# Kernel tuning notes

Measured on AMD Instinct MI355X. Metric: run time of the kernel, lower is better.

Reference implementation:

```python
import jax, jax.numpy as jnp
import numpy as np

LEVELS = [5023, 1256, 314, 79, 20]  # mesh vertex counts, fine -> coarse
T = 64        # number of audio frames
LATENT = 128  # latent_channels
S = 9         # spiral length
OUT_CH = [32, 64, 64, 128]


def setup_inputs() -> dict:
    key = jax.random.key(0)
    ks = list(jax.random.split(key, 40))
    nk = lambda: ks.pop()
    inp = {}
    inp["latent"] = jax.random.normal(nk(), (T, LATENT), jnp.float32)
    inp["actor"] = jax.random.normal(nk(), (LEVELS[0], 3), jnp.float32)
    # spiral indices per mesh level (levels 0..3 carry SpiralConvs)
    for l in range(4):
        n = LEVELS[l]
        inp[f"spiral{l}"] = jax.random.randint(nk(), (n, S), 0, n)
    # sparse up-transforms: level l+1 (coarse) -> level l (fine), ~3 nnz per fine vertex
    for l in range(4):
        nf, nc = LEVELS[l], LEVELS[l + 1]
        nnz = 3 * nf
        inp[f"up{l}_rows"] = jax.random.randint(nk(), (nnz,), 0, nf)
        inp[f"up{l}_cols"] = jax.random.randint(nk(), (nnz,), 0, nc)
        inp[f"up{l}_vals"] = jax.random.uniform(nk(), (nnz,), jnp.float32)
    def lin(k, od, idim):
        scale = np.sqrt(2.0 / (od + idim)).astype(np.float32)  # xavier-uniform-ish std
        return jax.random.normal(k, (od, idim), jnp.float32) * scale
    # de_layers[0]: Linear(latent -> num_vert * out_channels[-1])
    inp["W0"] = lin(nk(), LEVELS[4] * OUT_CH[-1], LATENT)
    inp["b0"] = jnp.zeros((LEVELS[4] * OUT_CH[-1],), jnp.float32)
    # SpiralDeblock convs (coarse -> fine): 128->128, 128->64, 64->64, 64->32
    inp["W1"] = lin(nk(), 128, 128 * S); inp["b1"] = jnp.zeros((128,), jnp.float32)
    inp["W2"] = lin(nk(), 64, 128 * S);  inp["b2"] = jnp.zeros((64,), jnp.float32)
    inp["W3"] = lin(nk(), 64, 64 * S);   inp["b3"] = jnp.zeros((64,), jnp.float32)
    inp["W4"] = lin(nk(), 32, 64 * S);   inp["b4"] = jnp.zeros((32,), jnp.float32)
    # final SpiralConv 32 -> 3 (init=True in torch zeros it; use small randn for testing)
    inp["Wf"] = lin(nk(), 3, 32 * S) * 0.1
    inp["bf"] = jnp.zeros((3,), jnp.float32)
    return inp


def spiral_conv(x, idx, W, b):
    # x: [T, n_in, C]; idx: [n, S] -> gather spiral neighborhoods, flatten, linear
    t, n = x.shape[0], idx.shape[0]
    g = x[:, idx.reshape(-1), :].reshape(t, n, -1)  # [T, n, S*C]
    return g @ W.T + b


def pool(x, rows, cols, vals, n_out):
    # sparse up-transform: out[:, rows] += x[:, cols] * vals  (scatter-add)
    g = x[:, cols, :] * vals[None, :, None]  # [T, nnz, C]
    return jnp.zeros((x.shape[0], n_out, x.shape[2]), x.dtype).at[:, rows].add(g)


def reference(latent, actor, spiral0, spiral1, spiral2, spiral3,
              up0_rows, up0_cols, up0_vals, up1_rows, up1_cols, up1_vals,
              up2_rows, up2_cols, up2_vals, up3_rows, up3_cols, up3_vals,
              W0, b0, W1, b1, W2, b2, W3, b3, W4, b4, Wf, bf):
    t = latent.shape[0]
    x = (latent @ W0.T + b0).reshape(t, LEVELS[4], OUT_CH[-1])  # [T, 20, 128]
    x = jax.nn.elu(spiral_conv(pool(x, up3_rows, up3_cols, up3_vals, LEVELS[3]), spiral3, W1, b1))
    x = jax.nn.elu(spiral_conv(pool(x, up2_rows, up2_cols, up2_vals, LEVELS[2]), spiral2, W2, b2))
    x = jax.nn.elu(spiral_conv(pool(x, up1_rows, up1_cols, up1_vals, LEVELS[1]), spiral1, W3, b3))
    x = jax.nn.elu(spiral_conv(pool(x, up0_rows, up0_cols, up0_vals, LEVELS[0]), spiral0, W4, b4))
    x = spiral_conv(x, spiral0, Wf, bf)  # [T, 5023, 3]
    return x + actor[None]  # per-frame offsets added to neutral actor mesh
```

## Files before the change

### kernel.cpp

```cpp
#include <hip/hip_runtime.h>
#include <hip/hip_bf16.h>

#define T_FRAMES 64

typedef __bf16 bf16x8 __attribute__((ext_vector_type(8)));
typedef __bf16 bf16x4 __attribute__((ext_vector_type(4)));
typedef float f32x4 __attribute__((ext_vector_type(4)));

#define NNZ0 15069
#define NNZ1 3768
#define NNZ2 942
#define NNZ3 237
#define N0 5023
#define N1 1256
#define N2 314
#define N3 79
#define N4 20


__global__ __launch_bounds__(256) void linear0_kernel(
    const float* __restrict__ latent, const float* __restrict__ W0,
    const float* __restrict__ b0, __bf16* __restrict__ out) {
  int id = blockIdx.x * 256 + threadIdx.x;
  if (id >= 64 * 2560) return;
  int j = id % 2560;
  int t = id / 2560;
  const float* lrow = latent + t * 128;
  const float* wrow = W0 + j * 128;
  float acc = b0[j];
#pragma unroll 8
  for (int k = 0; k < 128; ++k) acc = fmaf(lrow[k], wrow[k], acc);
  out[((size_t)(j >> 7) * 64 + t) * 128 + (j & 127)] = (__bf16)acc;
}

__global__ __launch_bounds__(256) void cvt_all_kernel(
    const float* __restrict__ W1, const float* __restrict__ W2,
    const float* __restrict__ W3, const float* __restrict__ W4,
    const float* __restrict__ Wf, __bf16* __restrict__ o) {
  int i = blockIdx.x * 256 + threadIdx.x;
  if (i < 147456) { o[i] = (__bf16)W1[i]; return; }
  if (i < 221184) { o[i] = (__bf16)W2[i - 147456]; return; }
  if (i < 258048) { o[i] = (__bf16)W3[i - 221184]; return; }
  if (i < 276480) { o[i] = (__bf16)W4[i - 258048]; return; }
  if (i < 281088) {
    int j = i - 276480;
    o[i] = (j / 288 < 3) ? (__bf16)Wf[j] : (__bf16)0.f;
  }
}

__global__ __launch_bounds__(256) void csr_count_kernel(
    const int* __restrict__ r0, const int* __restrict__ r1,
    const int* __restrict__ r2, const int* __restrict__ r3,
    int* __restrict__ c0, int* __restrict__ c1,
    int* __restrict__ c2, int* __restrict__ c3) {
  int i = blockIdx.x * 256 + threadIdx.x;
  if (i < NNZ0) atomicAdd(&c0[r0[i]], 1);
  else if (i < NNZ0 + NNZ1) atomicAdd(&c1[r1[i - NNZ0]], 1);
  else if (i < NNZ0 + NNZ1 + NNZ2) atomicAdd(&c2[r2[i - NNZ0 - NNZ1]], 1);
  else if (i < NNZ0 + NNZ1 + NNZ2 + NNZ3) atomicAdd(&c3[r3[i - NNZ0 - NNZ1 - NNZ2]], 1);
}

__global__ __launch_bounds__(256) void csr_scan_kernel(
    const int* __restrict__ c0, const int* __restrict__ c1,
    const int* __restrict__ c2, const int* __restrict__ c3,
    int* __restrict__ o0, int* __restrict__ o1,
    int* __restrict__ o2, int* __restrict__ o3,
    int* __restrict__ u0, int* __restrict__ u1,
    int* __restrict__ u2, int* __restrict__ u3) {
  const int b = blockIdx.x;
  const int* counts = b == 0 ? c0 : b == 1 ? c1 : b == 2 ? c2 : c3;
  int* off = b == 0 ? o0 : b == 1 ? o1 : b == 2 ? o2 : o3;
  int* cur = b == 0 ? u0 : b == 1 ? u1 : b == 2 ? u2 : u3;
  const int n = b == 0 ? N0 : b == 1 ? N1 : b == 2 ? N2 : N3;

  __shared__ int part[256];
  const int chunk = (n + 255) / 256;
  const int start = threadIdx.x * chunk;
  const int end = min(start + chunk, n);
  int s = 0;
  for (int i = start; i < end; ++i) s += counts[i];
  part[threadIdx.x] = s;
  __syncthreads();
  for (int d = 1; d < 256; d <<= 1) {
    int v = (threadIdx.x >= d) ? part[threadIdx.x - d] : 0;
    __syncthreads();
    part[threadIdx.x] += v;
    __syncthreads();
  }
  int run = (threadIdx.x == 0) ? 0 : part[threadIdx.x - 1];
  for (int i = start; i < end; ++i) {
    off[i] = run;
    cur[i] = run;
    run += counts[i];
  }
  if (threadIdx.x == 255) off[n] = run;
}

__global__ __launch_bounds__(256) void csr_bucket_kernel(
    const int* __restrict__ r0, const int* __restrict__ r1,
    const int* __restrict__ r2, const int* __restrict__ r3,
    const int* __restrict__ q0, const int* __restrict__ q1,
    const int* __restrict__ q2, const int* __restrict__ q3,
    const float* __restrict__ v0, const float* __restrict__ v1,
    const float* __restrict__ v2, const float* __restrict__ v3,
    int* __restrict__ u0, int* __restrict__ u1,
    int* __restrict__ u2, int* __restrict__ u3,
    int2* __restrict__ p0, int2* __restrict__ p1,
    int2* __restrict__ p2, int2* __restrict__ p3) {
  int i = blockIdx.x * 256 + threadIdx.x;
  if (i < NNZ0) {
    int p = atomicAdd(&u0[r0[i]], 1);
    p0[p] = make_int2(q0[i], __float_as_int(v0[i]));
  } else if (i < NNZ0 + NNZ1) {
    int e = i - NNZ0;
    int p = atomicAdd(&u1[r1[e]], 1);
    p1[p] = make_int2(q1[e], __float_as_int(v1[e]));
  } else if (i < NNZ0 + NNZ1 + NNZ2) {
    int e = i - NNZ0 - NNZ1;
    int p = atomicAdd(&u2[r2[e]], 1);
    p2[p] = make_int2(q2[e], __float_as_int(v2[e]));
  } else if (i < NNZ0 + NNZ1 + NNZ2 + NNZ3) {
    int e = i - NNZ0 - NNZ1 - NNZ2;
    int p = atomicAdd(&u3[r3[e]], 1);
    p3[p] = make_int2(q3[e], __float_as_int(v3[e]));
  }
}

template <int C, int TT>
__global__ __launch_bounds__(256) void pool_csr_kernel(
    const __bf16* __restrict__ x, const int* __restrict__ off,
    const int2* __restrict__ pk, __bf16* __restrict__ out, int n_out) {
  unsigned id = blockIdx.x * 256u + threadIdx.x;
  unsigned total = (unsigned)n_out * (T_FRAMES / TT) * C;
  if (id >= total) return;
  const int c = id % C;
  const unsigned rt = id / C;
  const int tb = rt % (T_FRAMES / TT);
  const int row = rt / (T_FRAMES / TT);

  const int o0 = off[row], o1 = off[row + 1];
  float acc[TT];
#pragma unroll
  for (int u = 0; u < TT; ++u) acc[u] = 0.f;

  for (int j = o0; j < o1; ++j) {
    const int2 rec = pk[j];
    const float val = __int_as_float(rec.y);
    const __bf16* xp = x + ((size_t)rec.x * T_FRAMES + tb * TT) * C + c;
#pragma unroll
    for (int u = 0; u < TT; ++u)
      acc[u] = fmaf(val, (float)xp[(size_t)u * C], acc[u]);
  }

  __bf16* op = out + ((size_t)row * T_FRAMES + tb * TT) * C + c;
#pragma unroll
  for (int u = 0; u < TT; ++u) op[(size_t)u * C] = (__bf16)acc[u];
}

template <int CIN, int COUT, int WV, int MT>
__global__ __launch_bounds__(WV * 64) void conv_mfma_kernel(
    const __bf16* __restrict__ x, const int* __restrict__ idx,
    const __bf16* __restrict__ Wb, const float* __restrict__ bias,
    __bf16* __restrict__ out) {
  constexpr int K = 9 * CIN;
  constexpr int KK = K / 32;
  constexpr int NT = COUT / 16;

  const int lane = threadIdx.x & 63;
  const int wid = threadIdx.x >> 6;
  const int v = blockIdx.x;
  const int tq0 = (blockIdx.y * WV + wid) * MT;
  const int col = lane & 15;
  const int kg = lane >> 4;

  size_t vbase[9];
#pragma unroll
  for (int s = 0; s < 9; ++s)
    vbase[s] = (size_t)idx[v * 9 + s] * (T_FRAMES * CIN);

  bf16x8 a[MT][KK];
#pragma unroll
  for (int mt = 0; mt < MT; ++mt) {
    const size_t trow = (size_t)(tq0 + mt) * 16 + col;
#pragma unroll
    for (int kk = 0; kk < KK; ++kk) {
      const int s = (kk * 32) / CIN;
      const int ci0 = (kk * 32) % CIN;
      a[mt][kk] = *(const bf16x8*)(x + vbase[s] + trow * CIN + ci0 + kg * 8);
    }
  }

  f32x4 acc[MT][NT];
#pragma unroll
  for (int nt = 0; nt < NT; ++nt) {
    float b = bias[nt * 16 + col];
#pragma unroll
    for (int mt = 0; mt < MT; ++mt) acc[mt][nt] = (f32x4){b, b, b, b};
  }

#pragma unroll
  for (int kk = 0; kk < KK; ++kk) {
#pragma unroll
    for (int nt = 0; nt < NT; ++nt) {
      bf16x8 bfr = *(const bf16x8*)(Wb + (size_t)(nt * 16 + col) * K + kk * 32 + kg * 8);
#pragma unroll
      for (int mt = 0; mt < MT; ++mt)
        acc[mt][nt] = __builtin_amdgcn_mfma_f32_16x16x32_bf16(a[mt][kk], bfr, acc[mt][nt], 0, 0, 0);
    }
  }

#pragma unroll
  for (int mt = 0; mt < MT; ++mt) {
#pragma unroll
    for (int j = 0; j < 4; ++j) {
      const size_t tr = (size_t)(tq0 + mt) * 16 + kg * 4 + j;
#pragma unroll
      for (int nt = 0; nt < NT; ++nt) {
        float aa = acc[mt][nt][j];
        aa = aa > 0.f ? aa : expm1f(aa);
        out[((size_t)v * T_FRAMES + tr) * COUT + nt * 16 + col] = (__bf16)aa;
      }
    }
  }
}

__global__ __launch_bounds__(256) void final_dense_kernel(
    const __bf16* __restrict__ z, const __bf16* __restrict__ Wfp,
    __bf16* __restrict__ Z) {
  const int lane = threadIdx.x & 63;
  const int wid = threadIdx.x >> 6;
  const int u = blockIdx.x;
  const int col = lane & 15;
  const int kg = lane >> 4;
  const size_t trow = (size_t)wid * 16 + col;

  const bf16x8 a = *(const bf16x8*)(z + ((size_t)u * T_FRAMES + trow) * 32 + kg * 8);

#pragma unroll
  for (int s = 0; s < 9; ++s) {
    const bf16x8 w = *(const bf16x8*)(Wfp + col * 288 + s * 32 + kg * 8);
    f32x4 acc = (f32x4){0.f, 0.f, 0.f, 0.f};
    acc = __builtin_amdgcn_mfma_f32_16x16x32_bf16(a, w, acc, 0, 0, 0);
    if (col < 4) {
#pragma unroll
      for (int j = 0; j < 4; ++j) {
        const size_t tr = (size_t)wid * 16 + kg * 4 + j;
        Z[(((size_t)u * 9 + s) * T_FRAMES + tr) * 4 + col] = (__bf16)acc[j];
      }
    }
  }
}

__global__ __launch_bounds__(256) void final_gather_kernel(
    const __bf16* __restrict__ Z, const int* __restrict__ idx,
    const float* __restrict__ bf3, const float* __restrict__ actor,
    float* __restrict__ out) {
  const unsigned id = blockIdx.x * 256u + threadIdx.x;
  if (id >= (unsigned)N0 * T_FRAMES) return;
  const int t = id & 63;
  const int v = id >> 6;

  float a0 = bf3[0], a1 = bf3[1], a2 = bf3[2];
#pragma unroll
  for (int s = 0; s < 9; ++s) {
    const int u = idx[v * 9 + s];
    const bf16x4 zz = *(const bf16x4*)(Z + (((size_t)u * 9 + s) * T_FRAMES + t) * 4);
    a0 += (float)zz[0];
    a1 += (float)zz[1];
    a2 += (float)zz[2];
  }
  float* op = out + ((size_t)t * N0 + v) * 3;
  op[0] = a0 + actor[v * 3 + 0];
  op[1] = a1 + actor[v * 3 + 1];
  op[2] = a2 + actor[v * 3 + 2];
}

extern "C" void kernel_launch(void* const* d_in, const int* in_sizes, int n_in_args,
                              void* d_out, int out_size, void* d_ws, size_t ws_size,
                              hipStream_t stream) {
  const float* latent = (const float*)d_in[0];
  const float* actor  = (const float*)d_in[1];
  const int* spiral0 = (const int*)d_in[2];
  const int* spiral1 = (const int*)d_in[3];
  const int* spiral2 = (const int*)d_in[4];
  const int* spiral3 = (const int*)d_in[5];
  const int* up0_rows = (const int*)d_in[6];
  const int* up0_cols = (const int*)d_in[7];
  const float* up0_vals = (const float*)d_in[8];
  const int* up1_rows = (const int*)d_in[9];
  const int* up1_cols = (const int*)d_in[10];
  const float* up1_vals = (const float*)d_in[11];
  const int* up2_rows = (const int*)d_in[12];
  const int* up2_cols = (const int*)d_in[13];
  const float* up2_vals = (const float*)d_in[14];
  const int* up3_rows = (const int*)d_in[15];
  const int* up3_cols = (const int*)d_in[16];
  const float* up3_vals = (const float*)d_in[17];
  const float* W0 = (const float*)d_in[18];
  const float* b0 = (const float*)d_in[19];
  const float* W1 = (const float*)d_in[20];
  const float* b1 = (const float*)d_in[21];
  const float* W2 = (const float*)d_in[22];
  const float* b2 = (const float*)d_in[23];
  const float* W3 = (const float*)d_in[24];
  const float* b3 = (const float*)d_in[25];
  const float* W4 = (const float*)d_in[26];
  const float* b4 = (const float*)d_in[27];
  const float* Wf = (const float*)d_in[28];
  const float* bf3 = (const float*)d_in[29];
  float* out = (float*)d_out;

  __bf16* poolbuf = (__bf16*)d_ws;
  __bf16* convout = poolbuf + 20574208;
  __bf16* wbuf = convout + 10287104;
  __bf16* W1b = wbuf;
  __bf16* W2b = W1b + 147456;
  __bf16* W3b = W2b + 73728;
  __bf16* W4b = W3b + 36864;
  __bf16* Wfp = W4b + 18432;
  int* csr = (int*)(wbuf + 281088);
  int* cnt0 = csr;            int* cnt1 = cnt0 + N0;   int* cnt2 = cnt1 + N1;   int* cnt3 = cnt2 + N2;
  int* off0 = csr + 6672;     int* off1 = off0 + N0+1; int* off2 = off1 + N1+1; int* off3 = off2 + N2+1;
  int* cur0 = csr + 13348;    int* cur1 = cur0 + N0;   int* cur2 = cur1 + N1;   int* cur3 = cur2 + N2;
  int2* pk0 = (int2*)(csr + 20020);
  int2* pk1 = pk0 + NNZ0;
  int2* pk2 = pk1 + NNZ1;
  int2* pk3 = pk2 + NNZ2;
  __bf16* Zbuf = poolbuf;

  hipMemsetAsync(cnt0, 0, 6672 * sizeof(int), stream);
  csr_count_kernel<<<(20016 + 255) / 256, 256, 0, stream>>>(
      up0_rows, up1_rows, up2_rows, up3_rows, cnt0, cnt1, cnt2, cnt3);
  csr_scan_kernel<<<4, 256, 0, stream>>>(cnt0, cnt1, cnt2, cnt3,
                                         off0, off1, off2, off3,
                                         cur0, cur1, cur2, cur3);
  csr_bucket_kernel<<<(20016 + 255) / 256, 256, 0, stream>>>(
      up0_rows, up1_rows, up2_rows, up3_rows,
      up0_cols, up1_cols, up2_cols, up3_cols,
      up0_vals, up1_vals, up2_vals, up3_vals,
      cur0, cur1, cur2, cur3, pk0, pk1, pk2, pk3);

  cvt_all_kernel<<<(281088 + 255) / 256, 256, 0, stream>>>(W1, W2, W3, W4, Wf, wbuf);

  linear0_kernel<<<(64 * 2560 + 255) / 256, 256, 0, stream>>>(latent, W0, b0, convout);

  pool_csr_kernel<128, 16><<<(N3 * 4 * 128 + 255) / 256, 256, 0, stream>>>(
      convout, off3, pk3, poolbuf, N3);
  conv_mfma_kernel<128, 128, 1, 1><<<dim3(N3, 4), 64, 0, stream>>>(
      poolbuf, spiral3, W1b, b1, convout);

  pool_csr_kernel<128, 16><<<(N2 * 4 * 128 + 255) / 256, 256, 0, stream>>>(
      convout, off2, pk2, poolbuf, N2);
  conv_mfma_kernel<128, 64, 1, 1><<<dim3(N2, 4), 64, 0, stream>>>(
      poolbuf, spiral2, W2b, b2, convout);

  pool_csr_kernel<64, 16><<<(N1 * 4 * 64 + 255) / 256, 256, 0, stream>>>(
      convout, off1, pk1, poolbuf, N1);
  conv_mfma_kernel<64, 64, 2, 2><<<dim3(N1, 1), 128, 0, stream>>>(
      poolbuf, spiral1, W3b, b3, convout);

  pool_csr_kernel<64, 16><<<(N0 * 4 * 64 + 255) / 256, 256, 0, stream>>>(
      convout, off0, pk0, poolbuf, N0);
  conv_mfma_kernel<64, 32, 2, 2><<<dim3(N0, 1), 128, 0, stream>>>(
      poolbuf, spiral0, W4b, b4, convout);

  final_dense_kernel<<<N0, 256, 0, stream>>>(convout, Wfp, Zbuf);
  final_gather_kernel<<<(N0 * T_FRAMES + 255) / 256, 256, 0, stream>>>(
      Zbuf, spiral0, bf3, actor, out);
}
```

Before: 407.3 us.

## Merge CSR build into one LDS kernel, fuse prep kernels, vectorize pooling

The memset plus three CSR kernels (count, scan, bucket) become a single kernel with one block per level, counting in shared memory, scanning, and bucketing there. The linear0 and weight-convert kernels are merged into one launch split by block index. The pooling kernel now has each thread handle 8 contiguous channels for one frame using 16-byte bf16x8 loads and stores, replacing scalar strided accesses over 16 frames. The aim is fewer launches and better memory coalescing, at the cost of serial CSR construction in only 4 blocks and about 20KB of LDS in that kernel.

Measured after the change: 430.6 us. 1.06x slower.

```diff
diff --git a/kernel.cpp b/kernel.cpp
--- a/kernel.cpp
+++ b/kernel.cpp
@@ -18,26 +18,25 @@
 #define N4 20
 
 
-__global__ __launch_bounds__(256) void linear0_kernel(
+__global__ __launch_bounds__(256) void prep_kernel(
     const float* __restrict__ latent, const float* __restrict__ W0,
-    const float* __restrict__ b0, __bf16* __restrict__ out) {
-  int id = blockIdx.x * 256 + threadIdx.x;
-  if (id >= 64 * 2560) return;
-  int j = id % 2560;
-  int t = id / 2560;
-  const float* lrow = latent + t * 128;
-  const float* wrow = W0 + j * 128;
-  float acc = b0[j];
-#pragma unroll 8
-  for (int k = 0; k < 128; ++k) acc = fmaf(lrow[k], wrow[k], acc);
-  out[((size_t)(j >> 7) * 64 + t) * 128 + (j & 127)] = (__bf16)acc;
-}
-
-__global__ __launch_bounds__(256) void cvt_all_kernel(
+    const float* __restrict__ b0, __bf16* __restrict__ out,
     const float* __restrict__ W1, const float* __restrict__ W2,
     const float* __restrict__ W3, const float* __restrict__ W4,
     const float* __restrict__ Wf, __bf16* __restrict__ o) {
-  int i = blockIdx.x * 256 + threadIdx.x;
+  if (blockIdx.x < 640) {
+    int id = blockIdx.x * 256 + threadIdx.x;
+    int j = id % 2560;
+    int t = id / 2560;
+    const float* lrow = latent + t * 128;
+    const float* wrow = W0 + j * 128;
+    float acc = b0[j];
+#pragma unroll 8
+    for (int k = 0; k < 128; ++k) acc = fmaf(lrow[k], wrow[k], acc);
+    out[((size_t)(j >> 7) * 64 + t) * 128 + (j & 127)] = (__bf16)acc;
+    return;
+  }
+  int i = (blockIdx.x - 640) * 256 + threadIdx.x;
   if (i < 147456) { o[i] = (__bf16)W1[i]; return; }
   if (i < 221184) { o[i] = (__bf16)W2[i - 147456]; return; }
   if (i < 258048) { o[i] = (__bf16)W3[i - 221184]; return; }
@@ -48,37 +47,39 @@
   }
 }
 
-__global__ __launch_bounds__(256) void csr_count_kernel(
+__global__ __launch_bounds__(256) void csr_build_kernel(
     const int* __restrict__ r0, const int* __restrict__ r1,
     const int* __restrict__ r2, const int* __restrict__ r3,
-    int* __restrict__ c0, int* __restrict__ c1,
-    int* __restrict__ c2, int* __restrict__ c3) {
-  int i = blockIdx.x * 256 + threadIdx.x;
-  if (i < NNZ0) atomicAdd(&c0[r0[i]], 1);
-  else if (i < NNZ0 + NNZ1) atomicAdd(&c1[r1[i - NNZ0]], 1);
-  else if (i < NNZ0 + NNZ1 + NNZ2) atomicAdd(&c2[r2[i - NNZ0 - NNZ1]], 1);
-  else if (i < NNZ0 + NNZ1 + NNZ2 + NNZ3) atomicAdd(&c3[r3[i - NNZ0 - NNZ1 - NNZ2]], 1);
-}
-
-__global__ __launch_bounds__(256) void csr_scan_kernel(
-    const int* __restrict__ c0, const int* __restrict__ c1,
-    const int* __restrict__ c2, const int* __restrict__ c3,
+    const int* __restrict__ q0, const int* __restrict__ q1,
+    const int* __restrict__ q2, const int* __restrict__ q3,
+    const float* __restrict__ v0, const float* __restrict__ v1,
+    const float* __restrict__ v2, const float* __restrict__ v3,
     int* __restrict__ o0, int* __restrict__ o1,
     int* __restrict__ o2, int* __restrict__ o3,
-    int* __restrict__ u0, int* __restrict__ u1,
-    int* __restrict__ u2, int* __restrict__ u3) {
+    int2* __restrict__ p0, int2* __restrict__ p1,
+    int2* __restrict__ p2, int2* __restrict__ p3) {
   const int b = blockIdx.x;
-  const int* counts = b == 0 ? c0 : b == 1 ? c1 : b == 2 ? c2 : c3;
+  const int* rows = b == 0 ? r0 : b == 1 ? r1 : b == 2 ? r2 : r3;
+  const int* cols = b == 0 ? q0 : b == 1 ? q1 : b == 2 ? q2 : q3;
+  const float* vals = b == 0 ? v0 : b == 1 ? v1 : b == 2 ? v2 : v3;
   int* off = b == 0 ? o0 : b == 1 ? o1 : b == 2 ? o2 : o3;
-  int* cur = b == 0 ? u0 : b == 1 ? u1 : b == 2 ? u2 : u3;
+  int2* pk = b == 0 ? p0 : b == 1 ? p1 : b == 2 ? p2 : p3;
   const int n = b == 0 ? N0 : b == 1 ? N1 : b == 2 ? N2 : N3;
-
+  const int nnz = b == 0 ? NNZ0 : b == 1 ? NNZ1 : b == 2 ? NNZ2 : NNZ3;
+
+  __shared__ int cnt[N0];
   __shared__ int part[256];
+
+  for (int i = threadIdx.x; i < n; i += 256) cnt[i] = 0;
+  __syncthreads();
+  for (int e = threadIdx.x; e < nnz; e += 256) atomicAdd(&cnt[rows[e]], 1);
+  __syncthreads();
+
   const int chunk = (n + 255) / 256;
   const int start = threadIdx.x * chunk;
   const int end = min(start + chunk, n);
   int s = 0;
-  for (int i = start; i < end; ++i) s += counts[i];
+  for (int i = start; i < end; ++i) s += cnt[i];
   part[threadIdx.x] = s;
   __syncthreads();
   for (int d = 1; d < 256; d <<= 1) {
@@ -89,72 +90,49 @@
   }
   int run = (threadIdx.x == 0) ? 0 : part[threadIdx.x - 1];
   for (int i = start; i < end; ++i) {
+    int c = cnt[i];
     off[i] = run;
-    cur[i] = run;
-    run += counts[i];
+    cnt[i] = run;
+    run += c;
   }
   if (threadIdx.x == 255) off[n] = run;
-}
-
-__global__ __launch_bounds__(256) void csr_bucket_kernel(
-    const int* __restrict__ r0, const int* __restrict__ r1,
-    const int* __restrict__ r2, const int* __restrict__ r3,
-    const int* __restrict__ q0, const int* __restrict__ q1,
-    const int* __restrict__ q2, const int* __restrict__ q3,
-    const float* __restrict__ v0, const float* __restrict__ v1,
-    const float* __restrict__ v2, const float* __restrict__ v3,
-    int* __restrict__ u0, int* __restrict__ u1,
-    int* __restrict__ u2, int* __restrict__ u3,
-    int2* __restrict__ p0, int2* __restrict__ p1,
-    int2* __restrict__ p2, int2* __restrict__ p3) {
-  int i = blockIdx.x * 256 + threadIdx.x;
-  if (i < NNZ0) {
-    int p = atomicAdd(&u0[r0[i]], 1);
-    p0[p] = make_int2(q0[i], __float_as_int(v0[i]));
-  } else if (i < NNZ0 + NNZ1) {
-    int e = i - NNZ0;
-    int p = atomicAdd(&u1[r1[e]], 1);
-    p1[p] = make_int2(q1[e], __float_as_int(v1[e]));
-  } else if (i < NNZ0 + NNZ1 + NNZ2) {
-    int e = i - NNZ0 - NNZ1;
-    int p = atomicAdd(&u2[r2[e]], 1);
-    p2[p] = make_int2(q2[e], __float_as_int(v2[e]));
-  } else if (i < NNZ0 + NNZ1 + NNZ2 + NNZ3) {
-    int e = i - NNZ0 - NNZ1 - NNZ2;
-    int p = atomicAdd(&u3[r3[e]], 1);
-    p3[p] = make_int2(q3[e], __float_as_int(v3[e]));
-  }
-}
-
-template <int C, int TT>
+  __syncthreads();
+
+  for (int e = threadIdx.x; e < nnz; e += 256) {
+    int p = atomicAdd(&cnt[rows[e]], 1);
+    pk[p] = make_int2(cols[e], __float_as_int(vals[e]));
+  }
+}
+
+template <int C>
 __global__ __launch_bounds__(256) void pool_csr_kernel(
     const __bf16* __restrict__ x, const int* __restrict__ off,
     const int2* __restrict__ pk, __bf16* __restrict__ out, int n_out) {
+  constexpr int C8 = C / 8;
   unsigned id = blockIdx.x * 256u + threadIdx.x;
-  unsigned total = (unsigned)n_out * (T_FRAMES / TT) * C;
+  unsigned total = (unsigned)n_out * T_FRAMES * C8;
   if (id >= total) return;
-  const int c = id % C;
-  const unsigned rt = id / C;
-  const int tb = rt % (T_FRAMES / TT);
-  const int row = rt / (T_FRAMES / TT);
+  const int c8 = id % C8;
+  const int t = (id / C8) % T_FRAMES;
+  const int row = id / (C8 * T_FRAMES);
 
   const int o0 = off[row], o1 = off[row + 1];
-  float acc[TT];
-#pragma unroll
-  for (int u = 0; u < TT; ++u) acc[u] = 0.f;
+  float acc[8];
+#pragma unroll
+  for (int u = 0; u < 8; ++u) acc[u] = 0.f;
 
   for (int j = o0; j < o1; ++j) {
     const int2 rec = pk[j];
     const float val = __int_as_float(rec.y);
-    const __bf16* xp = x + ((size_t)rec.x * T_FRAMES + tb * TT) * C + c;
-#pragma unroll
-    for (int u = 0; u < TT; ++u)
-      acc[u] = fmaf(val, (float)xp[(size_t)u * C], acc[u]);
-  }
-
-  __bf16* op = out + ((size_t)row * T_FRAMES + tb * TT) * C + c;
-#pragma unroll
-  for (int u = 0; u < TT; ++u) op[(size_t)u * C] = (__bf16)acc[u];
+    const bf16x8 xv = *(const bf16x8*)(x + ((size_t)rec.x * T_FRAMES + t) * C + c8 * 8);
+#pragma unroll
+    for (int u = 0; u < 8; ++u) acc[u] = fmaf(val, (float)xv[u], acc[u]);
+  }
+
+  bf16x8 ov;
+#pragma unroll
+  for (int u = 0; u < 8; ++u) ov[u] = (__bf16)acc[u];
+  *(bf16x8*)(out + ((size_t)row * T_FRAMES + t) * C + c8 * 8) = ov;
 }
 
 template <int CIN, int COUT, int WV, int MT>
@@ -319,47 +297,39 @@
   __bf16* W4b = W3b + 36864;
   __bf16* Wfp = W4b + 18432;
   int* csr = (int*)(wbuf + 281088);
-  int* cnt0 = csr;            int* cnt1 = cnt0 + N0;   int* cnt2 = cnt1 + N1;   int* cnt3 = cnt2 + N2;
-  int* off0 = csr + 6672;     int* off1 = off0 + N0+1; int* off2 = off1 + N1+1; int* off3 = off2 + N2+1;
-  int* cur0 = csr + 13348;    int* cur1 = cur0 + N0;   int* cur2 = cur1 + N1;   int* cur3 = cur2 + N2;
-  int2* pk0 = (int2*)(csr + 20020);
+  int* off0 = csr;            int* off1 = off0 + N0 + 1;
+  int* off2 = off1 + N1 + 1;  int* off3 = off2 + N2 + 1;
+  int2* pk0 = (int2*)(csr + 6676);
   int2* pk1 = pk0 + NNZ0;
   int2* pk2 = pk1 + NNZ1;
   int2* pk3 = pk2 + NNZ2;
   __bf16* Zbuf = poolbuf;
 
-  hipMemsetAsync(cnt0, 0, 6672 * sizeof(int), stream);
-  csr_count_kernel<<<(20016 + 255) / 256, 256, 0, stream>>>(
-      up0_rows, up1_rows, up2_rows, up3_rows, cnt0, cnt1, cnt2, cnt3);
-  csr_scan_kernel<<<4, 256, 0, stream>>>(cnt0, cnt1, cnt2, cnt3,
-                                         off0, off1, off2, off3,
-                                         cur0, cur1, cur2, cur3);
-  csr_bucket_kernel<<<(20016 + 255) / 256, 256, 0, stream>>>(
+  csr_build_kernel<<<4, 256, 0, stream>>>(
       up0_rows, up1_rows, up2_rows, up3_rows,
       up0_cols, up1_cols, up2_cols, up3_cols,
       up0_vals, up1_vals, up2_vals, up3_vals,
-      cur0, cur1, cur2, cur3, pk0, pk1, pk2, pk3);
-
-  cvt_all_kernel<<<(281088 + 255) / 256, 256, 0, stream>>>(W1, W2, W3, W4, Wf, wbuf);
-
-  linear0_kernel<<<(64 * 2560 + 255) / 256, 256, 0, stream>>>(latent, W0, b0, convout);
-
-  pool_csr_kernel<128, 16><<<(N3 * 4 * 128 + 255) / 256, 256, 0, stream>>>(
+      off0, off1, off2, off3, pk0, pk1, pk2, pk3);
+
+  prep_kernel<<<640 + (281088 + 255) / 256, 256, 0, stream>>>(
+      latent, W0, b0, convout, W1, W2, W3, W4, Wf, wbuf);
+
+  pool_csr_kernel<128><<<(N3 * 64 * 16 + 255) / 256, 256, 0, stream>>>(
       convout, off3, pk3, poolbuf, N3);
   conv_mfma_kernel<128, 128, 1, 1><<<dim3(N3, 4), 64, 0, stream>>>(
       poolbuf, spiral3, W1b, b1, convout);
 
-  pool_csr_kernel<128, 16><<<(N2 * 4 * 128 + 255) / 256, 256, 0, stream>>>(
+  pool_csr_kernel<128><<<(N2 * 64 * 16 + 255) / 256, 256, 0, stream>>>(
       convout, off2, pk2, poolbuf, N2);
   conv_mfma_kernel<128, 64, 1, 1><<<dim3(N2, 4), 64, 0, stream>>>(
       poolbuf, spiral2, W2b, b2, convout);
 
-  pool_csr_kernel<64, 16><<<(N1 * 4 * 64 + 255) / 256, 256, 0, stream>>>(
+  pool_csr_kernel<64><<<(N1 * 64 * 8 + 255) / 256, 256, 0, stream>>>(
       convout, off1, pk1, poolbuf, N1);
   conv_mfma_kernel<64, 64, 2, 2><<<dim3(N1, 1), 128, 0, stream>>>(
       poolbuf, spiral1, W3b, b3, convout);
 
-  pool_csr_kernel<64, 16><<<(N0 * 4 * 64 + 255) / 256, 256, 0, stream>>>(
+  pool_csr_kernel<64><<<(N0 * 64 * 8 + 255) / 256, 256, 0, stream>>>(
       convout, off0, pk0, poolbuf, N0);
   conv_mfma_kernel<64, 32, 2, 2><<<dim3(N0, 1), 128, 0, stream>>>(
       poolbuf, spiral0, W4b, b4, convout);
```
